# Optimization experiments

Measured on AMD Instinct MI355X. Metric: run time of the kernel, lower is better.

The kernel has to match this reference:

```python
import jax, jax.numpy as jnp
import numpy as np
from jax import lax

# Model / data dims (match init_kwargs / input_specs)
B, SEQ_LEN, IN_DIM, HID, TGT, PRED_LEN = 64, 1024, 128, 256, 128, 192
NUM_SCALES, TOP_K, KS = 2, 3, 3
DN = ('NCHW', 'OIHW', 'NCHW')


def avg_pool1d(x):
    # stride-2 average pool over last axis: [B,C,T] -> [B,C,T//2]
    b, c, t = x.shape
    return x[..., : (t // 2) * 2].reshape(b, c, t // 2, 2).mean(-1)


def dsconv2d(z, dw_w, dw_b, pw_w, pw_b):
    # depthwise 3x3 (groups=C_in, SAME pad) + pointwise 1x1 (C_in -> HID)
    c = z.shape[1]
    y = lax.conv_general_dilated(z, dw_w, (1, 1), 'SAME',
                                 feature_group_count=c, dimension_numbers=DN)
    y = y + dw_b[None, :, None, None]
    y = lax.conv_general_dilated(y, pw_w, (1, 1), 'SAME', dimension_numbers=DN)
    return y + pw_b[None, :, None, None]


def mean_amplitudes(xm):
    # xm: [B,C,T]; mean |rfft| over batch and channels, DC component zeroed
    a = jnp.abs(jnp.fft.rfft(xm, axis=-1)).mean(axis=(0, 1))
    return a.at[0].set(0.0)


def topk_freqs(xm, k):
    # concrete (eager) top-k frequency indices -> python ints (mirrors .item())
    amps = mean_amplitudes(xm)
    idx = np.asarray(lax.top_k(amps, k)[1])
    return [max(1, int(i)) for i in idx]


def setup_inputs() -> dict:
    key = jax.random.key(0)
    ks = jax.random.split(key, 8)
    s = 0.05
    return {
        'x': jax.random.normal(ks[0], (B, SEQ_LEN, IN_DIM), jnp.float32),
        'dw_w': jax.random.normal(ks[1], (IN_DIM, 1, KS, KS), jnp.float32) * s,
        'dw_b': jnp.zeros((IN_DIM,), jnp.float32),
        'pw_w': jax.random.normal(ks[2], (HID, IN_DIM, 1, 1), jnp.float32) * s,
        'pw_b': jnp.zeros((HID,), jnp.float32),
        'w_t0': jax.random.normal(ks[3], (PRED_LEN, SEQ_LEN), jnp.float32) * s,
        'b_t0': jnp.zeros((PRED_LEN,), jnp.float32),
        'w_t1': jax.random.normal(ks[4], (PRED_LEN, SEQ_LEN // 2), jnp.float32) * s,
        'b_t1': jnp.zeros((PRED_LEN,), jnp.float32),
        'w_t2': jax.random.normal(ks[5], (PRED_LEN, SEQ_LEN // 4), jnp.float32) * s,
        'b_t2': jnp.zeros((PRED_LEN,), jnp.float32),
        'w_ch': jax.random.normal(ks[6], (TGT, HID), jnp.float32) * s,
        'b_ch': jnp.zeros((TGT,), jnp.float32),
        'scale_logits': jnp.zeros((NUM_SCALES + 1,), jnp.float32),
    }


def _forward(x, dw_w, dw_b, pw_w, pw_b, time_ws, time_bs, w_ch, b_ch,
             scale_logits, freqs_per_scale):
    x_ct = jnp.transpose(x, (0, 2, 1))  # [B,C,T]
    scales = [x_ct]
    for _ in range(NUM_SCALES):
        scales.append(avg_pool1d(scales[-1]))
    sw = jax.nn.softmax(scale_logits) * float(NUM_SCALES + 1)
    y_sum = 0.0
    for m, xm in enumerate(scales):
        t = xm.shape[-1]
        amps = mean_amplitudes(xm)
        freqs = freqs_per_scale[m]
        wk = jax.nn.softmax(amps[jnp.array(freqs)])  # softmax over top-k amps
        fused = 0.0
        for k, f in enumerate(freqs):
            p = t // f                      # period (python int)
            rows = -(-t // p)               # ceil(t / p)
            pad = rows * p - t
            z = jnp.pad(xm, ((0, 0), (0, 0), (0, pad)))
            z = z.reshape(xm.shape[0], xm.shape[1], rows, p)  # 1D -> 2D grid
            y2 = dsconv2d(z, dw_w, dw_b, pw_w, pw_b)          # [B,HID,rows,p]
            y1 = y2.reshape(y2.shape[0], HID, rows * p)[..., :t]
            fused = fused + wk[k] * y1
        # dropout is identity in eval mode; l_m == time_projs[m].in_features here
        pred = jnp.einsum('bhl,pl->bph', fused, time_ws[m]) + time_bs[m][None, :, None]
        y_m = jnp.einsum('bph,oh->bpo', pred, w_ch) + b_ch
        y_sum = y_sum + sw[m] * y_m
    # residual: seq_len >= pred_len, input_dim == target_dim -> plain slice add
    return y_sum + x[:, -PRED_LEN:, :]


def reference(x, dw_w, dw_b, pw_w, pw_b, w_t0, b_t0, w_t1, b_t1, w_t2, b_t2,
              w_ch, b_ch, scale_logits):
    scales = [jnp.transpose(x, (0, 2, 1))]
    for _ in range(NUM_SCALES):
        scales.append(avg_pool1d(scales[-1]))
    freqs_per_scale = [topk_freqs(xm, TOP_K) for xm in scales]
    return _forward(x, dw_w, dw_b, pw_w, pw_b, [w_t0, w_t1, w_t2],
                    [b_t0, b_t1, b_t2], w_ch, b_ch, scale_logits, freqs_per_scale)
```

## Files before the change

### kernel.cpp

```cpp
#include <hip/hip_runtime.h>
#include <math.h>

#define NB   64
#define T0   1024
#define CIN  128
#define HID  256
#define TGT  128
#define PRED 192
#define NROWS (NB*CIN)
#define KTOT 1792

typedef __attribute__((ext_vector_type(4))) float f32x4;
typedef __attribute__((ext_vector_type(8))) short s16x8;

static const size_t XCT_OFF    = 0;
static const size_t S1_OFF     = 8388608;
static const size_t S2_OFF     = 12582912;
static const size_t P0_OFF     = 14680064;
static const size_t PARTS2_OFF = 15622144;
static const size_t META_OFF   = 15647104;
static const size_t W2T_OFF    = 15647168;
static const size_t PBS_OFF    = 15655360;
static const size_t WSUM_OFF   = 15655616;
static const size_t TB32_OFF   = 15656192;
static const size_t TB16_OFF   = 15659264;
static const size_t WTB_OFF    = 15660800;
static const size_t DWM_OFF    = 15832832;
static const size_t TP_OFF     = 23172864;

__device__ inline unsigned short f2bf(float x) {
    union { float f; unsigned u; } v; v.f = x;
    unsigned r = (v.u + 0x7FFFu + ((v.u >> 16) & 1u)) >> 16;
    return (unsigned short)r;
}
__device__ inline float bf2f(unsigned short u) {
    union { unsigned u; float f; } v; v.u = ((unsigned)u) << 16;
    return v.f;
}

__global__ __launch_bounds__(256) void front(const float* __restrict__ x,
        float* __restrict__ xct, float* __restrict__ s1, float* __restrict__ s2) {
    __shared__ float tile[32][33];
    int b = blockIdx.z;
    int t0 = blockIdx.x * 32, c0 = blockIdx.y * 32;
    int tx = threadIdx.x, ty = threadIdx.y;
#pragma unroll
    for (int i = 0; i < 4; i++) {
        int t = t0 + ty + i * 8, c = c0 + tx;
        tile[ty + i * 8][tx] = x[((size_t)b * T0 + t) * CIN + c];
    }
    __syncthreads();
#pragma unroll
    for (int i = 0; i < 4; i++) {
        int c = c0 + ty + i * 8, cc = ty + i * 8;
        xct[((size_t)b * CIN + c) * T0 + t0 + tx] = tile[tx][cc];
        if (tx < 16) {
            float v = 0.5f * (tile[2 * tx][cc] + tile[2 * tx + 1][cc]);
            s1[((size_t)b * CIN + c) * (T0 / 2) + t0 / 2 + tx] = v;
        }
        if (tx < 8) {
            float v = 0.25f * (tile[4 * tx][cc] + tile[4 * tx + 1][cc]
                             + tile[4 * tx + 2][cc] + tile[4 * tx + 3][cc]);
            s2[((size_t)b * CIN + c) * (T0 / 4) + t0 / 4 + tx] = v;
        }
    }
}

__device__ void prep_body(const float* __restrict__ w_ch,
        const float* __restrict__ pw_w, const float* __restrict__ pw_b,
        const float* __restrict__ wt0, const float* __restrict__ wt1,
        const float* __restrict__ wt2, const float* __restrict__ slog,
        unsigned short* __restrict__ w2ot, float* __restrict__ pbs,
        unsigned short* __restrict__ wtb, float* __restrict__ wsum) {
    int tid = threadIdx.x;
    int bx = blockIdx.x;
    if (bx >= 209) return;
    if (bx < 64) {
        int idx = bx * 256 + tid;
        int c = idx >> 7, o = idx & 127;
        float acc = 0.f;
        for (int h = 0; h < HID; h++) acc += w_ch[o * HID + h] * pw_w[h * CIN + c];
        w2ot[o * 128 + (c ^ ((o & 7) << 3))] = f2bf(acc);
        return;
    }
    if (bx == 64) {
        if (tid < 128) {
            float pb = 0.f, s = 0.f;
            for (int h = 0; h < HID; h++) {
                float w = w_ch[tid * HID + h];
                pb += w * pw_b[h]; s += w;
            }
            pbs[tid] = pb; pbs[128 + tid] = s;
        }
        return;
    }
    float s0l = slog[0], s1l = slog[1], s2l = slog[2];
    float mx = fmaxf(s0l, fmaxf(s1l, s2l));
    float e0 = expf(s0l - mx), e1 = expf(s1l - mx), e2 = expf(s2l - mx);
    float inv = 3.f / (e0 + e1 + e2);
    float swl[3] = {e0 * inv, e1 * inv, e2 * inv};

    int wid = (bx - 65) * 4 + (tid >> 6);
    int lane = tid & 63;
    const float* src; int T, p, m; int moff;
    if (wid < 192)      { m = 0; p = wid;       src = wt0; T = 1024; moff = 0; }
    else if (wid < 384) { m = 1; p = wid - 192; src = wt1; T = 512;  moff = 1024; }
    else                { m = 2; p = wid - 384; src = wt2; T = 256;  moff = 1536; }
    float swm = swl[m];
    const float* row = src + (size_t)p * T;
    unsigned short* dst = wtb + (size_t)p * KTOT + moff;
    float s = 0.f;
    for (int j = lane; j < T; j += 64) {
        float v = row[j] * swm; s += v; dst[j] = f2bf(v);
    }
#pragma unroll
    for (int d = 1; d < 64; d <<= 1) s += __shfl_xor(s, d);
    if (lane == 0) wsum[m * 192 + p] = s;
}

#define PHYS(i) ((i) + ((i) >> 5))
template<int LOGT>
__device__ __forceinline__ void fft_body(const float* __restrict__ xm,
        float* __restrict__ part, int pad,
        float* re, float* im, float* twc, float* tws, float* acc) {
    constexpr int T = 1 << LOGT;
    constexpr int F = T / 2;
    int tid = threadIdx.x;
    for (int j = tid; j < F; j += 256) {
        float s, c;
        sincosf(-6.283185307179586f * (float)j / (float)T, &s, &c);
        twc[PHYS(j)] = c; tws[PHYS(j)] = s;
    }
    for (int i = tid; i <= F; i += 256) acc[i] = 0.f;
    __syncthreads();

    int rowbase = blockIdx.x * 8;
    for (int pr = 0; pr < 4; pr++) {
        const float* row0 = xm + (size_t)(rowbase + 2 * pr) * T;
        const float* row1 = row0 + T;
        if (tid < T / 4) {
            int base = (LOGT > 2) ? (int)(__brev((unsigned)tid) >> (32 - (LOGT - 2))) : 0;
            float x0r = row0[base],             x0i = row1[base];
            float x1r = row0[base + T / 2],     x1i = row1[base + T / 2];
            float x2r = row0[base + T / 4],     x2i = row1[base + T / 4];
            float x3r = row0[base + 3 * T / 4], x3i = row1[base + 3 * T / 4];
            float ar = x0r + x1r, ai = x0i + x1i;
            float br = x0r - x1r, bi = x0i - x1i;
            float cr = x2r + x3r, ci = x2i + x3i;
            float dr = x2r - x3r, di = x2i - x3i;
            int o = 4 * tid;
            re[PHYS(o)]     = ar + cr;  im[PHYS(o)]     = ai + ci;
            re[PHYS(o + 2)] = ar - cr;  im[PHYS(o + 2)] = ai - ci;
            re[PHYS(o + 1)] = br + di;  im[PHYS(o + 1)] = bi - dr;
            re[PHYS(o + 3)] = br - di;  im[PHYS(o + 3)] = bi + dr;
        }
        __syncthreads();
        for (int s = 3; s + 1 <= LOGT; s += 2) {
            int mh = 1 << (s - 1);
            if (tid < T / 4) {
                int k  = tid & (mh - 1);
                int gq = tid >> (s - 1);
                int i0 = (gq << (s + 1)) + k;
                int iA = PHYS(i0), iB = PHYS(i0 + mh);
                int iC = PHYS(i0 + 2 * mh), iD = PHYS(i0 + 3 * mh);
                int t1 = PHYS(k << (LOGT - s));
                int t2 = PHYS(k << (LOGT - s - 1));
                int t3 = PHYS((k + mh) << (LOGT - s - 1));
                float w1r = twc[t1], w1i = tws[t1];
                float w2r = twc[t2], w2i = tws[t2];
                float w3r = twc[t3], w3i = tws[t3];
                float ar = re[iA], ai = im[iA];
                float br = re[iB], bi = im[iB];
                float cr = re[iC], ci = im[iC];
                float dr = re[iD], di = im[iD];
                float tbr = w1r * br - w1i * bi, tbi = w1r * bi + w1i * br;
                float tdr = w1r * dr - w1i * di, tdi = w1r * di + w1i * dr;
                float v0r = ar + tbr, v0i = ai + tbi;
                float v1r = ar - tbr, v1i = ai - tbi;
                float v2r = cr + tdr, v2i = ci + tdi;
                float v3r = cr - tdr, v3i = ci - tdi;
                float t2r = w2r * v2r - w2i * v2i, t2i = w2r * v2i + w2i * v2r;
                float t3r = w3r * v3r - w3i * v3i, t3i = w3r * v3i + w3i * v3r;
                re[iA] = v0r + t2r; im[iA] = v0i + t2i;
                re[iC] = v0r - t2r; im[iC] = v0i - t2i;
                re[iB] = v1r + t3r; im[iB] = v1i + t3i;
                re[iD] = v1r - t3r; im[iD] = v1i - t3i;
            }
            __syncthreads();
        }
        if (LOGT & 1) {
            constexpr int s = LOGT;
            int mh = 1 << (s - 1);
            if (tid < T / 2) {
                int k  = tid & (mh - 1);
                int i1 = PHYS(tid);
                int i2 = PHYS(tid + mh);
                int tw = PHYS(k);
                float wr = twc[tw], wi = tws[tw];
                float xr = re[i2], xi = im[i2];
                float tr = wr * xr - wi * xi;
                float ti = wr * xi + wi * xr;
                float ur = re[i1], ui = im[i1];
                re[i1] = ur + tr; im[i1] = ui + ti;
                re[i2] = ur - tr; im[i2] = ui - ti;
            }
            __syncthreads();
        }
        for (int f = tid; f <= F; f += 256) {
            if (f >= 1) {
                int mf = T - f;
                float rf = re[PHYS(f)], imf = im[PHYS(f)];
                float rm = re[PHYS(mf)], imm = im[PHYS(mf)];
                float m0 = sqrtf((rf + rm) * (rf + rm) + (imf - imm) * (imf - imm));
                float m1 = sqrtf((imf + imm) * (imf + imm) + (rf - rm) * (rf - rm));
                acc[f] += 0.5f * (m0 + m1);
            }
        }
        __syncthreads();
    }
    for (int f = tid; f <= F; f += 256)
        part[(size_t)blockIdx.x * pad + f] = acc[f];
}

__global__ __launch_bounds__(256) void fft_all(const float* __restrict__ xct,
        const float* __restrict__ s1, const float* __restrict__ s2,
        float* __restrict__ parts,
        const float* __restrict__ w_ch, const float* __restrict__ pw_w,
        const float* __restrict__ pw_b, const float* __restrict__ wt0,
        const float* __restrict__ wt1, const float* __restrict__ wt2,
        const float* __restrict__ slog,
        unsigned short* __restrict__ w2ot, float* __restrict__ pbs,
        unsigned short* __restrict__ wtb, float* __restrict__ wsum) {
    __shared__ float re[1056], im[1056], twc[528], tws[528], acc[513];
    int sc = blockIdx.y;
    if (sc == 3) {
        prep_body(w_ch, pw_w, pw_b, wt0, wt1, wt2, slog, w2ot, pbs, wtb, wsum);
        return;
    }
    if (sc == 0)
        fft_body<10>(xct, parts, 520, re, im, twc, tws, acc);
    else if (sc == 1)
        fft_body<9>(s1, parts + (size_t)1024 * 520, 264, re, im, twc, tws, acc);
    else
        fft_body<8>(s2, parts + (size_t)1024 * 520 + (size_t)1024 * 264, 136,
                    re, im, twc, tws, acc);
}

__global__ __launch_bounds__(256) void reduce_partA(const float* __restrict__ parts,
                                                    float* __restrict__ parts2) {
    const int PADs[3] = {520, 264, 136};
    const int Fs[3]   = {513, 257, 129};
    const size_t POFF[3] = {0, (size_t)1024 * 520, (size_t)1024 * 520 + (size_t)1024 * 264};
    int s  = blockIdx.y;
    int rs = blockIdx.z;
    int fl = threadIdx.x & 63;
    int rg = threadIdx.x >> 6;
    int f  = blockIdx.x * 64 + fl;
    bool valid = f < Fs[s];
    const float* base = parts + POFF[s];
    int pad = PADs[s];
    float sum = 0.f;
    if (valid) {
        int r0 = rs * 64 + rg * 16;
#pragma unroll
        for (int i = 0; i < 16; i++) sum += base[(size_t)(r0 + i) * pad + f];
    }
    __shared__ float red[256];
    red[threadIdx.x] = sum;
    __syncthreads();
    if (rg == 0 && valid) {
        float tot = red[fl] + red[fl + 64] + red[fl + 128] + red[fl + 192];
        parts2[(size_t)(s * 16 + rs) * 520 + f] = tot;
    }
}

__device__ inline float sum16(const float* __restrict__ p2, int m, int f) {
    const float* b = p2 + (size_t)m * 16 * 520 + f;
    float s = 0.f;
#pragma unroll
    for (int r = 0; r < 16; r++) s += b[r * 520];
    return s;
}

__device__ inline void ins3(float v, int i, float& b0, int& c0,
                            float& b1, int& c1, float& b2, int& c2) {
    bool g0 = (v > b0) || (v == b0 && i < c0);
    bool g1 = (v > b1) || (v == b1 && i < c1);
    bool g2 = (v > b2) || (v == b2 && i < c2);
    if (g0)      { b2 = b1; c2 = c1; b1 = b0; c1 = c0; b0 = v; c0 = i; }
    else if (g1) { b2 = b1; c2 = c1; b1 = v; c1 = i; }
    else if (g2) { b2 = v; c2 = i; }
}

__global__ __launch_bounds__(256) void meta_topk(const float* __restrict__ parts2,
                          const float* __restrict__ slog,
                          int* __restrict__ freqs, float* __restrict__ wk,
                          float* __restrict__ sw,
                          unsigned* __restrict__ tb32g, unsigned short* __restrict__ tb16g) {
    __shared__ float sv[12];
    __shared__ int   si[12];
    __shared__ int   sfr[3];
    const int Fs[3] = {513, 257, 129};
    const int Ts[3] = {1024, 512, 256};
    int m = blockIdx.x;
    int tid = threadIdx.x, lane = tid & 63, wv = tid >> 6;
    int F = Fs[m];
    float b0 = -1e30f, b1 = -1e30f, b2 = -1e30f;
    int   c0 = 0x7fffffff, c1 = 0x7fffffff, c2 = 0x7fffffff;
    for (int i = tid; i < F; i += 256) {
        float v = (i == 0) ? 0.f : sum16(parts2, m, i) * (1.f / 8192.f);
        ins3(v, i, b0, c0, b1, c1, b2, c2);
    }
#pragma unroll
    for (int d = 1; d < 64; d <<= 1) {
        float o0 = __shfl_xor(b0, d), o1 = __shfl_xor(b1, d), o2 = __shfl_xor(b2, d);
        int   i0 = __shfl_xor(c0, d), i1 = __shfl_xor(c1, d), i2 = __shfl_xor(c2, d);
        ins3(o0, i0, b0, c0, b1, c1, b2, c2);
        ins3(o1, i1, b0, c0, b1, c1, b2, c2);
        ins3(o2, i2, b0, c0, b1, c1, b2, c2);
    }
    if (lane == 0) {
        sv[wv * 3 + 0] = b0; si[wv * 3 + 0] = c0;
        sv[wv * 3 + 1] = b1; si[wv * 3 + 1] = c1;
        sv[wv * 3 + 2] = b2; si[wv * 3 + 2] = c2;
    }
    __syncthreads();
    if (tid == 0) {
        float d0 = sv[0], d1 = sv[1], d2 = sv[2];
        int   e0 = si[0], e1 = si[1], e2 = si[2];
        for (int q = 3; q < 12; q++) ins3(sv[q], si[q], d0, e0, d1, e1, d2, e2);
        int fr[3] = {max(1, e0), max(1, e1), max(1, e2)};
        float av[3];
#pragma unroll
        for (int i = 0; i < 3; i++) av[i] = sum16(parts2, m, fr[i]) * (1.f / 8192.f);
        float mx = fmaxf(av[0], fmaxf(av[1], av[2]));
        float x0 = expf(av[0] - mx), x1 = expf(av[1] - mx), x2 = expf(av[2] - mx);
        float inv = 1.f / (x0 + x1 + x2);
        freqs[m * 3 + 0] = fr[0]; freqs[m * 3 + 1] = fr[1]; freqs[m * 3 + 2] = fr[2];
        wk[m * 3 + 0] = x0 * inv; wk[m * 3 + 1] = x1 * inv; wk[m * 3 + 2] = x2 * inv;
        sfr[0] = fr[0]; sfr[1] = fr[1]; sfr[2] = fr[2];
        if (m == 0) {
            float s0 = slog[0], s1 = slog[1], s2 = slog[2];
            float mx2 = fmaxf(s0, fmaxf(s1, s2));
            float e0b = expf(s0 - mx2), e1b = expf(s1 - mx2), e2b = expf(s2 - mx2);
            float inv2 = 3.f / (e0b + e1b + e2b);
            sw[0] = e0b * inv2; sw[1] = e1b * inv2; sw[2] = e2b * inv2;
        }
    }
    __syncthreads();
    int Tm = Ts[m];
    int p0 = Tm / sfr[0], p1 = Tm / sfr[1], p2v = Tm / sfr[2];
    int S0 = (p0 + 2) | 1, S1 = (p1 + 2) | 1, S2v = (p2v + 2) | 1;
    int r0n = (Tm + p0 - 1) / p0, r1n = (Tm + p1 - 1) / p1;
    int off0 = 0;
    int off1 = (r0n + 2) * S0;
    int off2 = off1 + (r1n + 2) * S1;
    for (int l = tid; l < Tm; l += 256) {
        int ra = l / p0, ca = l - ra * p0;
        int rb = l / p1, cb = l - rb * p1;
        int rc = l / p2v, cc = l - rc * p2v;
        unsigned ba = off0 + (ra + 1) * S0 + ca + 1;
        unsigned bb = off1 + (rb + 1) * S1 + cb + 1;
        unsigned bc = off2 + (rc + 1) * S2v + cc + 1;
        tb32g[m * 1024 + l] = ba | (bb << 16);
        tb16g[m * 1024 + l] = (unsigned short)bc;
    }
}

template<int T>
__device__ __forceinline__ void dwmix_body(const float* __restrict__ xm,
        const float* __restrict__ dw_w, const float* __restrict__ dw_b,
        const int* __restrict__ freqs, const float* __restrict__ wkbuf,
        const unsigned* __restrict__ tb32g, const unsigned short* __restrict__ tb16g,
        int m, int moff, unsigned short* __restrict__ dwm, float* xs) {
    constexpr int NP = T / 256;
    int tid = threadIdx.x;
    int c = blockIdx.x, b = blockIdx.y;
    int S0, S1, S2; float wkv[3]; int tot;
    {
        int off = 0; int Sv[3];
#pragma unroll
        for (int k = 0; k < 3; k++) {
            int f = freqs[m * 3 + k];
            int p = T / f;
            int S = (p + 2) | 1;
            Sv[k] = S;
            int rows = (T + p - 1) / p;
            off += (rows + 2) * S;
            wkv[k] = wkbuf[m * 3 + k];
        }
        S0 = Sv[0]; S1 = Sv[1]; S2 = Sv[2]; tot = off;
    }
    for (int i = tid; i < tot; i += 256) xs[i] = 0.f;
    __syncthreads();
    const float* src = xm + ((size_t)b * CIN + c) * T;
    const unsigned* t32 = tb32g + m * 1024;
    const unsigned short* t16 = tb16g + m * 1024;
    unsigned w32r[NP]; int b2r[NP];
#pragma unroll
    for (int i = 0; i < NP; i++) {
        int l = i * 256 + tid;
        float xv = src[l];
        unsigned w32 = t32[l];
        int b2v = t16[l];
        w32r[i] = w32; b2r[i] = b2v;
        xs[w32 & 0xffff] = xv;
        xs[w32 >> 16]    = xv;
        xs[b2v]          = xv;
    }
    __syncthreads();

    float wk9[27];
#pragma unroll
    for (int k = 0; k < 3; k++)
#pragma unroll
        for (int q = 0; q < 9; q++) wk9[k * 9 + q] = wkv[k] * dw_w[c * 9 + q];
    float bias = dw_b[c];
    unsigned short* outp = dwm + (size_t)(b * CIN + c) * KTOT + moff;

#pragma unroll
    for (int i = 0; i < NP; i++) {
        unsigned w32 = w32r[i];
        const float* q0 = xs + (w32 & 0xffff);
        const float* q1 = xs + (w32 >> 16);
        const float* q2 = xs + b2r[i];
        float a0 = wk9[0] * q0[-S0 - 1] + wk9[1] * q0[-S0] + wk9[2] * q0[-S0 + 1]
                 + wk9[3] * q0[-1]      + wk9[4] * q0[0]   + wk9[5] * q0[1]
                 + wk9[6] * q0[S0 - 1]  + wk9[7] * q0[S0]  + wk9[8] * q0[S0 + 1];
        float a1 = wk9[9]  * q1[-S1 - 1] + wk9[10] * q1[-S1] + wk9[11] * q1[-S1 + 1]
                 + wk9[12] * q1[-1]      + wk9[13] * q1[0]   + wk9[14] * q1[1]
                 + wk9[15] * q1[S1 - 1]  + wk9[16] * q1[S1]  + wk9[17] * q1[S1 + 1];
        float a2 = wk9[18] * q2[-S2 - 1] + wk9[19] * q2[-S2] + wk9[20] * q2[-S2 + 1]
                 + wk9[21] * q2[-1]      + wk9[22] * q2[0]   + wk9[23] * q2[1]
                 + wk9[24] * q2[S2 - 1]  + wk9[25] * q2[S2]  + wk9[26] * q2[S2 + 1];
        outp[i * 256 + tid] = f2bf(bias + a0 + a1 + a2);
    }
}

__global__ __launch_bounds__(256) void dwmix_s0(const float* __restrict__ xct,
        const float* __restrict__ dw_w, const float* __restrict__ dw_b,
        const int* __restrict__ freqs, const float* __restrict__ wkbuf,
        const unsigned* __restrict__ tb32g, const unsigned short* __restrict__ tb16g,
        unsigned short* __restrict__ dwm) {
    __shared__ float xs[7232];
    dwmix_body<1024>(xct, dw_w, dw_b, freqs, wkbuf, tb32g, tb16g, 0, 0, dwm, xs);
}

__global__ __launch_bounds__(256) void dwmix_s12(const float* __restrict__ s1,
        const float* __restrict__ s2,
        const float* __restrict__ dw_w, const float* __restrict__ dw_b,
        const int* __restrict__ freqs, const float* __restrict__ wkbuf,
        const unsigned* __restrict__ tb32g, const unsigned short* __restrict__ tb16g,
        unsigned short* __restrict__ dwm) {
    __shared__ float xs[3648];
    if (blockIdx.z == 0)
        dwmix_body<512>(s1, dw_w, dw_b, freqs, wkbuf, tb32g, tb16g, 1, 1024, dwm, xs);
    else
        dwmix_body<256>(s2, dw_w, dw_b, freqs, wkbuf, tb32g, tb16g, 2, 1536, dwm, xs);
}

__global__ __launch_bounds__(256) void tp_gemm(const unsigned short* __restrict__ A,
        const unsigned short* __restrict__ B, unsigned short* __restrict__ C) {
    __shared__ __align__(16) unsigned short As[64 * 72];
    __shared__ __align__(16) unsigned short Bs[64 * 72];
    int tid = threadIdx.x;
    int lane = tid & 63, wave = tid >> 6;
    int wm = (wave >> 1) * 32, wn = (wave & 1) * 32;
    int p0 = blockIdx.x * 64, n0 = blockIdx.y * 64;
    f32x4 acc[2][2];
#pragma unroll
    for (int i = 0; i < 2; i++)
#pragma unroll
        for (int j = 0; j < 2; j++) acc[i][j] = (f32x4){0.f, 0.f, 0.f, 0.f};

    int r = tid >> 2, seg = tid & 3;
    const unsigned short* ga = A + (size_t)(p0 + r) * KTOT + seg * 16;
    const unsigned short* gb = B + (size_t)(n0 + r) * KTOT + seg * 16;
    unsigned short* la = &As[r * 72 + seg * 16];
    unsigned short* lb = &Bs[r * 72 + seg * 16];
    int fr = lane & 15, fk = (lane >> 4) * 8;

    for (int k0 = 0; k0 < KTOT; k0 += 64) {
        __syncthreads();
        *(uint4*)la       = *(const uint4*)ga;
        *(uint4*)(la + 8) = *(const uint4*)(ga + 8);
        *(uint4*)lb       = *(const uint4*)gb;
        *(uint4*)(lb + 8) = *(const uint4*)(gb + 8);
        ga += 64; gb += 64;
        __syncthreads();
#pragma unroll
        for (int ks = 0; ks < 2; ks++) {
            int ko = ks * 32 + fk;
            s16x8 a0 = *(const s16x8*)&As[(wm + fr) * 72 + ko];
            s16x8 a1 = *(const s16x8*)&As[(wm + 16 + fr) * 72 + ko];
            s16x8 b0 = *(const s16x8*)&Bs[(wn + fr) * 72 + ko];
            s16x8 b1 = *(const s16x8*)&Bs[(wn + 16 + fr) * 72 + ko];
            acc[0][0] = __builtin_amdgcn_mfma_f32_16x16x32_bf16(a0, b0, acc[0][0], 0, 0, 0);
            acc[0][1] = __builtin_amdgcn_mfma_f32_16x16x32_bf16(a0, b1, acc[0][1], 0, 0, 0);
            acc[1][0] = __builtin_amdgcn_mfma_f32_16x16x32_bf16(a1, b0, acc[1][0], 0, 0, 0);
            acc[1][1] = __builtin_amdgcn_mfma_f32_16x16x32_bf16(a1, b1, acc[1][1], 0, 0, 0);
        }
    }
    int crow = (lane >> 4) * 4, ccol = lane & 15;
#pragma unroll
    for (int i = 0; i < 2; i++)
#pragma unroll
        for (int j = 0; j < 2; j++) {
            int col = n0 + wn + j * 16 + ccol;
#pragma unroll
            for (int reg = 0; reg < 4; reg++) {
                int row = p0 + wm + i * 16 + crow + reg;
                C[(size_t)row * 8192 + col] = f2bf(acc[i][j][reg]);
            }
        }
}

__global__ __launch_bounds__(256) void final_out(const float* __restrict__ x,
        const unsigned short* __restrict__ tp, const unsigned short* __restrict__ w2ot,
        const float* __restrict__ pbs, const float* __restrict__ wsum,
        const float* __restrict__ bt0, const float* __restrict__ bt1,
        const float* __restrict__ bt2, const float* __restrict__ b_ch,
        const float* __restrict__ swb, float* __restrict__ out) {
    __shared__ unsigned short w2s[128 * 128];
    __shared__ float tpsS[32][128];
    __shared__ float wsS[32], btS[32];
    int tid = threadIdx.x;
    int r0 = blockIdx.x * 32;
    float sw0 = swb[0], sw1 = swb[1], sw2 = swb[2];

#pragma unroll
    for (int i = 0; i < 8; i++)
        ((uint4*)w2s)[i * 256 + tid] = ((const uint4*)w2ot)[i * 256 + tid];
#pragma unroll
    for (int it = 0; it < 2; it++) {
        int idx = tid + it * 256;
        int rr = idx >> 4, u = idx & 15;
        int r = r0 + rr;
        int b2 = r / 192, p2 = r - b2 * 192;
        size_t base = (size_t)p2 * 8192 + (size_t)b2 * 128 + u * 8;
        uint4 q0 = *(const uint4*)&tp[base];
        const unsigned* a0 = (const unsigned*)&q0;
        float o8[8];
#pragma unroll
        for (int w = 0; w < 4; w++) {
            o8[2 * w]     = bf2f(a0[w] & 0xffff);
            o8[2 * w + 1] = bf2f(a0[w] >> 16);
        }
        *(float4*)&tpsS[rr][u * 8]     = *(float4*)&o8[0];
        *(float4*)&tpsS[rr][u * 8 + 4] = *(float4*)&o8[4];
    }
    if (tid < 32) {
        int r = r0 + tid;
        int b2 = r / 192, p = r - b2 * 192;
        wsS[tid] = wsum[p] + wsum[192 + p] + wsum[384 + p];
        btS[tid] = sw0 * bt0[p] + sw1 * bt1[p] + sw2 * bt2[p];
    }
    __syncthreads();

    int o = tid & 127, half = tid >> 7;
    int rbase = half * 16;
    float pbv  = pbs[o];
    float schv = pbs[128 + o];
    float bchv = (sw0 + sw1 + sw2) * b_ch[o];
    float acc[16];
#pragma unroll
    for (int rr = 0; rr < 16; rr++) acc[rr] = 0.f;

#pragma unroll 2
    for (int cb8 = 0; cb8 < 16; cb8++) {
        uint4 wv = *(const uint4*)&w2s[o * 128 + ((cb8 ^ (o & 7)) << 3)];
        const unsigned* aw = (const unsigned*)&wv;
        float wf[8];
#pragma unroll
        for (int w = 0; w < 4; w++) {
            wf[2 * w]     = bf2f(aw[w] & 0xffff);
            wf[2 * w + 1] = bf2f(aw[w] >> 16);
        }
        int cc = cb8 * 8;
#pragma unroll
        for (int rr = 0; rr < 16; rr++) {
            const float* tr = &tpsS[rbase + rr][cc];
            float4 t0 = *(const float4*)tr;
            float4 t1 = *(const float4*)(tr + 4);
            acc[rr] += wf[0] * t0.x + wf[1] * t0.y + wf[2] * t0.z + wf[3] * t0.w
                     + wf[4] * t1.x + wf[5] * t1.y + wf[6] * t1.z + wf[7] * t1.w;
        }
    }
#pragma unroll
    for (int rr = 0; rr < 16; rr++) {
        int r = r0 + rbase + rr;
        int b2 = r / 192, p = r - b2 * 192;
        float res = x[((size_t)b2 * T0 + (T0 - PRED) + p) * CIN + o];
        out[(size_t)r * TGT + o] = res + acc[rr] + pbv * wsS[rbase + rr]
                                 + schv * btS[rbase + rr] + bchv;
    }
}

extern "C" void kernel_launch(void* const* d_in, const int* in_sizes, int n_in,
                              void* d_out, int out_size, void* d_ws, size_t ws_size,
                              hipStream_t stream) {
    const float* x    = (const float*)d_in[0];
    const float* dw_w = (const float*)d_in[1];
    const float* dw_b = (const float*)d_in[2];
    const float* pw_w = (const float*)d_in[3];
    const float* pw_b = (const float*)d_in[4];
    const float* wt0  = (const float*)d_in[5];
    const float* bt0  = (const float*)d_in[6];
    const float* wt1  = (const float*)d_in[7];
    const float* bt1  = (const float*)d_in[8];
    const float* wt2  = (const float*)d_in[9];
    const float* bt2  = (const float*)d_in[10];
    const float* w_ch = (const float*)d_in[11];
    const float* b_ch = (const float*)d_in[12];
    const float* slog = (const float*)d_in[13];
    float* out = (float*)d_out;
    float* ws  = (float*)d_ws;

    float* xct    = ws + XCT_OFF;
    float* s1b    = ws + S1_OFF;
    float* s2b    = ws + S2_OFF;
    float* parts  = ws + P0_OFF;
    float* parts2 = ws + PARTS2_OFF;
    int*   freqs  = (int*)(ws + META_OFF);
    float* wkb    = ws + META_OFF + 16;
    float* swb    = ws + META_OFF + 32;
    unsigned short* w2tb = (unsigned short*)(ws + W2T_OFF);
    float* pbs    = ws + PBS_OFF;
    float* wsumb  = ws + WSUM_OFF;
    unsigned*       tb32g = (unsigned*)(ws + TB32_OFF);
    unsigned short* tb16g = (unsigned short*)(ws + TB16_OFF);
    unsigned short* wtb  = (unsigned short*)(ws + WTB_OFF);
    unsigned short* dwm  = (unsigned short*)(ws + DWM_OFF);
    unsigned short* tpb  = (unsigned short*)(ws + TP_OFF);

    front<<<dim3(32, 4, NB), dim3(32, 8, 1), 0, stream>>>(x, xct, s1b, s2b);
    fft_all<<<dim3(1024, 4), 256, 0, stream>>>(xct, s1b, s2b, parts,
                                               w_ch, pw_w, pw_b, wt0, wt1, wt2, slog,
                                               w2tb, pbs, wtb, wsumb);
    reduce_partA<<<dim3(9, 3, 16), 256, 0, stream>>>(parts, parts2);
    meta_topk<<<3, 256, 0, stream>>>(parts2, slog, freqs, wkb, swb, tb32g, tb16g);
    dwmix_s0<<<dim3(CIN, NB), 256, 0, stream>>>(xct, dw_w, dw_b, freqs, wkb,
                                                tb32g, tb16g, dwm);
    dwmix_s12<<<dim3(CIN, NB, 2), 256, 0, stream>>>(s1b, s2b, dw_w, dw_b, freqs, wkb,
                                                    tb32g, tb16g, dwm);
    tp_gemm<<<dim3(3, 128), 256, 0, stream>>>(wtb, dwm, tpb);
    final_out<<<384, 256, 0, stream>>>(x, tpb, w2tb, pbs, wsumb,
                                       bt0, bt1, bt2, b_ch, swb, out);
}
```

Measured before the change: 194.6 us.

## Batch two complex FFTs per pass and split top-k reduction into parallel stage

The FFT block now packs four real rows into two complex FFTs computed side by side in doubled shared buffers. This halves the number of barrier-separated passes per block and reuses each twiddle load for both FFTs. Separately, the 16-way partial-sum reduction and per-chunk top-3 selection move into a new multi-block kernel, so meta_topk only merges 27 candidates. The cost is double the shared memory for the FFT, which may lower occupancy, and one extra kernel launch.

```diff
diff --git a/kernel.cpp b/kernel.cpp
--- a/kernel.cpp
+++ b/kernel.cpp
@@ -19,14 +19,17 @@
 static const size_t P0_OFF     = 14680064;
 static const size_t PARTS2_OFF = 15622144;
 static const size_t META_OFF   = 15647104;
-static const size_t W2T_OFF    = 15647168;
-static const size_t PBS_OFF    = 15655360;
-static const size_t WSUM_OFF   = 15655616;
-static const size_t TB32_OFF   = 15656192;
-static const size_t TB16_OFF   = 15659264;
-static const size_t WTB_OFF    = 15660800;
-static const size_t DWM_OFF    = 15832832;
-static const size_t TP_OFF     = 23172864;
+static const size_t AMPS_OFF   = 15647168;
+static const size_t TOP3V_OFF  = 15648896;
+static const size_t TOP3I_OFF  = 15649024;
+static const size_t W2T_OFF    = 15649152;
+static const size_t PBS_OFF    = 15657344;
+static const size_t WSUM_OFF   = 15657600;
+static const size_t TB32_OFF   = 15658176;
+static const size_t TB16_OFF   = 15661248;
+static const size_t WTB_OFF    = 15662784;
+static const size_t DWM_OFF    = 15834816;
+static const size_t TP_OFF     = 23174848;
 
 __device__ inline unsigned short f2bf(float x) {
     union { float f; unsigned u; } v; v.f = x;
@@ -119,6 +122,7 @@
 }
 
 #define PHYS(i) ((i) + ((i) >> 5))
+#define OB 1056
 template<int LOGT>
 __device__ __forceinline__ void fft_body(const float* __restrict__ xm,
         float* __restrict__ part, int pad,
@@ -135,24 +139,42 @@
     __syncthreads();
 
     int rowbase = blockIdx.x * 8;
-    for (int pr = 0; pr < 4; pr++) {
-        const float* row0 = xm + (size_t)(rowbase + 2 * pr) * T;
-        const float* row1 = row0 + T;
+    for (int pr = 0; pr < 2; pr++) {
+        const float* a0p = xm + (size_t)(rowbase + 4 * pr) * T;
+        const float* a1p = a0p + T;
+        const float* b0p = a0p + 2 * (size_t)T;
+        const float* b1p = a0p + 3 * (size_t)T;
         if (tid < T / 4) {
-            int base = (LOGT > 2) ? (int)(__brev((unsigned)tid) >> (32 - (LOGT - 2))) : 0;
-            float x0r = row0[base],             x0i = row1[base];
-            float x1r = row0[base + T / 2],     x1i = row1[base + T / 2];
-            float x2r = row0[base + T / 4],     x2i = row1[base + T / 4];
-            float x3r = row0[base + 3 * T / 4], x3i = row1[base + 3 * T / 4];
-            float ar = x0r + x1r, ai = x0i + x1i;
-            float br = x0r - x1r, bi = x0i - x1i;
-            float cr = x2r + x3r, ci = x2i + x3i;
-            float dr = x2r - x3r, di = x2i - x3i;
+            int base = (int)(__brev((unsigned)tid) >> (32 - (LOGT - 2)));
             int o = 4 * tid;
-            re[PHYS(o)]     = ar + cr;  im[PHYS(o)]     = ai + ci;
-            re[PHYS(o + 2)] = ar - cr;  im[PHYS(o + 2)] = ai - ci;
-            re[PHYS(o + 1)] = br + di;  im[PHYS(o + 1)] = bi - dr;
-            re[PHYS(o + 3)] = br - di;  im[PHYS(o + 3)] = bi + dr;
+            {
+                float x0r = a0p[base],             x0i = a1p[base];
+                float x1r = a0p[base + T / 2],     x1i = a1p[base + T / 2];
+                float x2r = a0p[base + T / 4],     x2i = a1p[base + T / 4];
+                float x3r = a0p[base + 3 * T / 4], x3i = a1p[base + 3 * T / 4];
+                float ar = x0r + x1r, ai = x0i + x1i;
+                float br = x0r - x1r, bi = x0i - x1i;
+                float cr = x2r + x3r, ci = x2i + x3i;
+                float dr = x2r - x3r, di = x2i - x3i;
+                re[PHYS(o)]     = ar + cr;  im[PHYS(o)]     = ai + ci;
+                re[PHYS(o + 2)] = ar - cr;  im[PHYS(o + 2)] = ai - ci;
+                re[PHYS(o + 1)] = br + di;  im[PHYS(o + 1)] = bi - dr;
+                re[PHYS(o + 3)] = br - di;  im[PHYS(o + 3)] = bi + dr;
+            }
+            {
+                float x0r = b0p[base],             x0i = b1p[base];
+                float x1r = b0p[base + T / 2],     x1i = b1p[base + T / 2];
+                float x2r = b0p[base + T / 4],     x2i = b1p[base + T / 4];
+                float x3r = b0p[base + 3 * T / 4], x3i = b1p[base + 3 * T / 4];
+                float ar = x0r + x1r, ai = x0i + x1i;
+                float br = x0r - x1r, bi = x0i - x1i;
+                float cr = x2r + x3r, ci = x2i + x3i;
+                float dr = x2r - x3r, di = x2i - x3i;
+                re[OB + PHYS(o)]     = ar + cr;  im[OB + PHYS(o)]     = ai + ci;
+                re[OB + PHYS(o + 2)] = ar - cr;  im[OB + PHYS(o + 2)] = ai - ci;
+                re[OB + PHYS(o + 1)] = br + di;  im[OB + PHYS(o + 1)] = bi - dr;
+                re[OB + PHYS(o + 3)] = br - di;  im[OB + PHYS(o + 3)] = bi + dr;
+            }
         }
         __syncthreads();
         for (int s = 3; s + 1 <= LOGT; s += 2) {
@@ -169,51 +191,65 @@
                 float w1r = twc[t1], w1i = tws[t1];
                 float w2r = twc[t2], w2i = tws[t2];
                 float w3r = twc[t3], w3i = tws[t3];
-                float ar = re[iA], ai = im[iA];
-                float br = re[iB], bi = im[iB];
-                float cr = re[iC], ci = im[iC];
-                float dr = re[iD], di = im[iD];
-                float tbr = w1r * br - w1i * bi, tbi = w1r * bi + w1i * br;
-                float tdr = w1r * dr - w1i * di, tdi = w1r * di + w1i * dr;
-                float v0r = ar + tbr, v0i = ai + tbi;
-                float v1r = ar - tbr, v1i = ai - tbi;
-                float v2r = cr + tdr, v2i = ci + tdi;
-                float v3r = cr - tdr, v3i = ci - tdi;
-                float t2r = w2r * v2r - w2i * v2i, t2i = w2r * v2i + w2i * v2r;
-                float t3r = w3r * v3r - w3i * v3i, t3i = w3r * v3i + w3i * v3r;
-                re[iA] = v0r + t2r; im[iA] = v0i + t2i;
-                re[iC] = v0r - t2r; im[iC] = v0i - t2i;
-                re[iB] = v1r + t3r; im[iB] = v1i + t3i;
-                re[iD] = v1r - t3r; im[iD] = v1i - t3i;
+#pragma unroll
+                for (int ff = 0; ff < 2; ff++) {
+                    int off = ff * OB;
+                    float ar = re[off + iA], ai = im[off + iA];
+                    float br = re[off + iB], bi = im[off + iB];
+                    float cr = re[off + iC], ci = im[off + iC];
+                    float dr = re[off + iD], di = im[off + iD];
+                    float tbr = w1r * br - w1i * bi, tbi = w1r * bi + w1i * br;
+                    float tdr = w1r * dr - w1i * di, tdi = w1r * di + w1i * dr;
+                    float v0r = ar + tbr, v0i = ai + tbi;
+                    float v1r = ar - tbr, v1i = ai - tbi;
+                    float v2r = cr + tdr, v2i = ci + tdi;
+                    float v3r = cr - tdr, v3i = ci - tdi;
+                    float t2r = w2r * v2r - w2i * v2i, t2i = w2r * v2i + w2i * v2r;
+                    float t3r = w3r * v3r - w3i * v3i, t3i = w3r * v3i + w3i * v3r;
+                    re[off + iA] = v0r + t2r; im[off + iA] = v0i + t2i;
+                    re[off + iC] = v0r - t2r; im[off + iC] = v0i - t2i;
+                    re[off + iB] = v1r + t3r; im[off + iB] = v1i + t3i;
+                    re[off + iD] = v1r - t3r; im[off + iD] = v1i - t3i;
+                }
             }
             __syncthreads();
         }
         if (LOGT & 1) {
-            constexpr int s = LOGT;
-            int mh = 1 << (s - 1);
+            int mh = 1 << (LOGT - 1);
             if (tid < T / 2) {
                 int k  = tid & (mh - 1);
                 int i1 = PHYS(tid);
                 int i2 = PHYS(tid + mh);
                 int tw = PHYS(k);
                 float wr = twc[tw], wi = tws[tw];
-                float xr = re[i2], xi = im[i2];
-                float tr = wr * xr - wi * xi;
-                float ti = wr * xi + wi * xr;
-                float ur = re[i1], ui = im[i1];
-                re[i1] = ur + tr; im[i1] = ui + ti;
-                re[i2] = ur - tr; im[i2] = ui - ti;
+#pragma unroll
+                for (int ff = 0; ff < 2; ff++) {
+                    int off = ff * OB;
+                    float xr = re[off + i2], xi = im[off + i2];
+                    float tr = wr * xr - wi * xi;
+                    float ti = wr * xi + wi * xr;
+                    float ur = re[off + i1], ui = im[off + i1];
+                    re[off + i1] = ur + tr; im[off + i1] = ui + ti;
+                    re[off + i2] = ur - tr; im[off + i2] = ui - ti;
+                }
             }
             __syncthreads();
         }
         for (int f = tid; f <= F; f += 256) {
             if (f >= 1) {
                 int mf = T - f;
-                float rf = re[PHYS(f)], imf = im[PHYS(f)];
-                float rm = re[PHYS(mf)], imm = im[PHYS(mf)];
-                float m0 = sqrtf((rf + rm) * (rf + rm) + (imf - imm) * (imf - imm));
-                float m1 = sqrtf((imf + imm) * (imf + imm) + (rf - rm) * (rf - rm));
-                acc[f] += 0.5f * (m0 + m1);
+                int pf = PHYS(f), pm = PHYS(mf);
+                float s = 0.f;
+#pragma unroll
+                for (int ff = 0; ff < 2; ff++) {
+                    int off = ff * OB;
+                    float rf = re[off + pf], imf = im[off + pf];
+                    float rm = re[off + pm], imm = im[off + pm];
+                    float m0 = sqrtf((rf + rm) * (rf + rm) + (imf - imm) * (imf - imm));
+                    float m1 = sqrtf((imf + imm) * (imf + imm) + (rf - rm) * (rf - rm));
+                    s += 0.5f * (m0 + m1);
+                }
+                acc[f] += s;
             }
         }
         __syncthreads();
@@ -231,7 +267,7 @@
         const float* __restrict__ slog,
         unsigned short* __restrict__ w2ot, float* __restrict__ pbs,
         unsigned short* __restrict__ wtb, float* __restrict__ wsum) {
-    __shared__ float re[1056], im[1056], twc[528], tws[528], acc[513];
+    __shared__ float re[2112], im[2112], twc[528], tws[528], acc[513];
     int sc = blockIdx.y;
     if (sc == 3) {
         prep_body(w_ch, pw_w, pw_b, wt0, wt1, wt2, slog, w2ot, pbs, wtb, wsum);
@@ -274,14 +310,6 @@
     }
 }
 
-__device__ inline float sum16(const float* __restrict__ p2, int m, int f) {
-    const float* b = p2 + (size_t)m * 16 * 520 + f;
-    float s = 0.f;
-#pragma unroll
-    for (int r = 0; r < 16; r++) s += b[r * 520];
-    return s;
-}
-
 __device__ inline void ins3(float v, int i, float& b0, int& c0,
                             float& b1, int& c1, float& b2, int& c2) {
     bool g0 = (v > b0) || (v == b0 && i < c0);
@@ -292,47 +320,65 @@
     else if (g2) { b2 = v; c2 = i; }
 }
 
-__global__ __launch_bounds__(256) void meta_topk(const float* __restrict__ parts2,
+__global__ __launch_bounds__(256) void reduce_partB(const float* __restrict__ parts2,
+        float* __restrict__ amps, float* __restrict__ top3v, int* __restrict__ top3i) {
+    const int Fs[3] = {513, 257, 129};
+    int s  = blockIdx.y;
+    int fx = blockIdx.x;
+    int fl = threadIdx.x & 63;
+    int rg = threadIdx.x >> 6;
+    int f  = fx * 64 + fl;
+    bool valid = f < Fs[s];
+    float sum = 0.f;
+    if (valid) {
+        const float* b = parts2 + (size_t)(s * 16 + rg * 4) * 520 + f;
+#pragma unroll
+        for (int r = 0; r < 4; r++) sum += b[r * 520];
+    }
+    __shared__ float red[256];
+    red[threadIdx.x] = sum;
+    __syncthreads();
+    if (rg == 0) {
+        float tot = red[fl] + red[fl + 64] + red[fl + 128] + red[fl + 192];
+        float v = valid ? ((f == 0) ? 0.f : tot * (1.f / 8192.f)) : -1e30f;
+        if (valid) amps[s * 576 + f] = v;
+        float b0 = v, b1 = -1e30f, b2 = -1e30f;
+        int   c0 = f, c1 = 0x7fffffff, c2 = 0x7fffffff;
+#pragma unroll
+        for (int d = 1; d < 64; d <<= 1) {
+            float o0 = __shfl_xor(b0, d), o1 = __shfl_xor(b1, d), o2 = __shfl_xor(b2, d);
+            int   i0 = __shfl_xor(c0, d), i1 = __shfl_xor(c1, d), i2 = __shfl_xor(c2, d);
+            ins3(o0, i0, b0, c0, b1, c1, b2, c2);
+            ins3(o1, i1, b0, c0, b1, c1, b2, c2);
+            ins3(o2, i2, b0, c0, b1, c1, b2, c2);
+        }
+        if (fl == 0) {
+            int base = (s * 9 + fx) * 3;
+            top3v[base] = b0; top3v[base + 1] = b1; top3v[base + 2] = b2;
+            top3i[base] = c0; top3i[base + 1] = c1; top3i[base + 2] = c2;
+        }
+    }
+}
+
+__global__ __launch_bounds__(256) void meta_topk(const float* __restrict__ amps,
+                          const float* __restrict__ top3v, const int* __restrict__ top3i,
                           const float* __restrict__ slog,
                           int* __restrict__ freqs, float* __restrict__ wk,
                           float* __restrict__ sw,
                           unsigned* __restrict__ tb32g, unsigned short* __restrict__ tb16g) {
-    __shared__ float sv[12];
-    __shared__ int   si[12];
-    __shared__ int   sfr[3];
-    const int Fs[3] = {513, 257, 129};
+    __shared__ int sfr[3];
     const int Ts[3] = {1024, 512, 256};
     int m = blockIdx.x;
-    int tid = threadIdx.x, lane = tid & 63, wv = tid >> 6;
-    int F = Fs[m];
-    float b0 = -1e30f, b1 = -1e30f, b2 = -1e30f;
-    int   c0 = 0x7fffffff, c1 = 0x7fffffff, c2 = 0x7fffffff;
-    for (int i = tid; i < F; i += 256) {
-        float v = (i == 0) ? 0.f : sum16(parts2, m, i) * (1.f / 8192.f);
-        ins3(v, i, b0, c0, b1, c1, b2, c2);
-    }
-#pragma unroll
-    for (int d = 1; d < 64; d <<= 1) {
-        float o0 = __shfl_xor(b0, d), o1 = __shfl_xor(b1, d), o2 = __shfl_xor(b2, d);
-        int   i0 = __shfl_xor(c0, d), i1 = __shfl_xor(c1, d), i2 = __shfl_xor(c2, d);
-        ins3(o0, i0, b0, c0, b1, c1, b2, c2);
-        ins3(o1, i1, b0, c0, b1, c1, b2, c2);
-        ins3(o2, i2, b0, c0, b1, c1, b2, c2);
-    }
-    if (lane == 0) {
-        sv[wv * 3 + 0] = b0; si[wv * 3 + 0] = c0;
-        sv[wv * 3 + 1] = b1; si[wv * 3 + 1] = c1;
-        sv[wv * 3 + 2] = b2; si[wv * 3 + 2] = c2;
-    }
-    __syncthreads();
+    int tid = threadIdx.x;
     if (tid == 0) {
-        float d0 = sv[0], d1 = sv[1], d2 = sv[2];
-        int   e0 = si[0], e1 = si[1], e2 = si[2];
-        for (int q = 3; q < 12; q++) ins3(sv[q], si[q], d0, e0, d1, e1, d2, e2);
-        int fr[3] = {max(1, e0), max(1, e1), max(1, e2)};
+        float b0 = -1e30f, b1 = -1e30f, b2 = -1e30f;
+        int   c0 = 0x7fffffff, c1 = 0x7fffffff, c2 = 0x7fffffff;
+        for (int q = 0; q < 27; q++)
+            ins3(top3v[m * 27 + q], top3i[m * 27 + q], b0, c0, b1, c1, b2, c2);
+        int fr[3] = {max(1, c0), max(1, c1), max(1, c2)};
         float av[3];
 #pragma unroll
-        for (int i = 0; i < 3; i++) av[i] = sum16(parts2, m, fr[i]) * (1.f / 8192.f);
+        for (int i = 0; i < 3; i++) av[i] = amps[m * 576 + fr[i]];
         float mx = fmaxf(av[0], fmaxf(av[1], av[2]));
         float x0 = expf(av[0] - mx), x1 = expf(av[1] - mx), x2 = expf(av[2] - mx);
         float inv = 1.f / (x0 + x1 + x2);
@@ -624,6 +670,9 @@
     int*   freqs  = (int*)(ws + META_OFF);
     float* wkb    = ws + META_OFF + 16;
     float* swb    = ws + META_OFF + 32;
+    float* ampsb  = ws + AMPS_OFF;
+    float* top3v  = ws + TOP3V_OFF;
+    int*   top3i  = (int*)(ws + TOP3I_OFF);
     unsigned short* w2tb = (unsigned short*)(ws + W2T_OFF);
     float* pbs    = ws + PBS_OFF;
     float* wsumb  = ws + WSUM_OFF;
@@ -638,7 +687,9 @@
                                                w_ch, pw_w, pw_b, wt0, wt1, wt2, slog,
                                                w2tb, pbs, wtb, wsumb);
     reduce_partA<<<dim3(9, 3, 16), 256, 0, stream>>>(parts, parts2);
-    meta_topk<<<3, 256, 0, stream>>>(parts2, slog, freqs, wkb, swb, tb32g, tb16g);
+    reduce_partB<<<dim3(9, 3), 256, 0, stream>>>(parts2, ampsb, top3v, top3i);
+    meta_topk<<<3, 256, 0, stream>>>(ampsb, top3v, top3i, slog, freqs, wkb, swb,
+                                     tb32g, tb16g);
     dwmix_s0<<<dim3(CIN, NB), 256, 0, stream>>>(xct, dw_w, dw_b, freqs, wkb,
                                                 tb32g, tb16g, dwm);
     dwmix_s12<<<dim3(CIN, NB, 2), 256, 0, stream>>>(s1b, s2b, dw_w, dw_b, freqs, wkb,
```

Result: slower. 202.7 us (+4.1%).
